# Optimization experiments

Measured on AMD Instinct MI355X. Metric: run time of the kernel, lower is better.

## Reference

```python
import jax, jax.numpy as jnp
import numpy as np

EPS = 0.1
SHAPE = (1, 1, 96, 96)  # [B, C, H, W]


def setup_inputs() -> dict:
    key = jax.random.key(0)
    x = jax.random.normal(key, SHAPE, dtype=jnp.float32)
    return {"x": x}


def reference(x):
    eps = EPS
    B, C, H, W = x.shape
    N = C * H * W  # max possible new error terms; buffer grows to 1 + N slots

    # clip the eps-ball into [0, 1]: bias shifts, error radius shrinks
    r_low = jax.nn.relu(eps - x) * 0.5
    r_high = jax.nn.relu(x - (1.0 - eps)) * 0.5
    bias = x + r_low - r_high                  # zonotope center, [B,C,H,W]
    err = eps - r_low - r_high                 # per-pixel error magnitude

    ef = err.reshape(N)
    cond = ef >= 0                             # which pixels get an error term
    # stream compaction: k-th true condition -> error-term slot 1+k (slot 0 = bias)
    slot = jnp.cumsum(cond.astype(jnp.int32))  # 1-based compacted index
    err_idx = jnp.where(cond, slot, N + 1)     # out-of-range -> dropped

    f, i, j = jnp.unravel_index(jnp.arange(N), (C, H, W))

    zono = jnp.zeros((B, 1 + N, C, H, W), dtype=x.dtype)
    zono = zono.at[0, 0].set(bias[0])
    zono = zono.at[0, err_idx, f, i, j].set(ef, mode='drop')
    return zono
```

## Files before the change

### kernel.cpp

```cpp
#include <hip/hip_runtime.h>

#define NPIX 9216
#define NROWS (NPIX + 1)
#define ROW4 (NPIX / 4)
#define EPSV 0.1f

typedef float f32x4 __attribute__((ext_vector_type(4)));

__global__ __launch_bounds__(1024) void finish_kernel(const float* __restrict__ x,
                                                      float* __restrict__ out) {
    __shared__ int wsum[16];
    const int tid  = threadIdx.x;
    const int lane = tid & 63;
    const int wid  = tid >> 6;
    const int base = tid * 9;

    float e_loc[9];
    int   c_loc[9];
    int   cnt = 0;
#pragma unroll
    for (int k = 0; k < 9; ++k) {
        const float xv     = x[base + k];
        const float r_low  = fmaxf(EPSV - xv, 0.0f) * 0.5f;
        const float r_high = fmaxf(xv - (1.0f - EPSV), 0.0f) * 0.5f;
        const float e      = EPSV - r_low - r_high;
        e_loc[k] = e;
        c_loc[k] = (e >= 0.0f) ? 1 : 0;
        cnt += c_loc[k];
    }

    int v = cnt;
#pragma unroll
    for (int off = 1; off < 64; off <<= 1) {
        const int t = __shfl_up(v, off, 64);
        if (lane >= off) v += t;
    }
    if (lane == 63) wsum[wid] = v;
    __syncthreads();

    int woff = 0;
#pragma unroll
    for (int w = 0; w < 16; ++w) woff += (w < wid) ? wsum[w] : 0;

    int slot = woff + v - cnt;
#pragma unroll
    for (int k = 0; k < 9; ++k) {
        if (c_loc[k]) {
            ++slot;
            out[(long long)slot * NPIX + (base + k)] = e_loc[k];
        }
    }

    const f32x4* x4 = reinterpret_cast<const f32x4*>(x);
    f32x4* o4 = reinterpret_cast<f32x4*>(out);
#pragma unroll
    for (int it = 0; it < 3; ++it) {
        const int c4 = tid + it * 1024;
        if (c4 < ROW4) {
            const f32x4 xv = x4[c4];
            f32x4 o;
#pragma unroll
            for (int d = 0; d < 4; ++d) {
                const float vv = xv[d];
                o[d] = vv + fmaxf(EPSV - vv, 0.0f) * 0.5f
                          - fmaxf(vv - (1.0f - EPSV), 0.0f) * 0.5f;
            }
            o4[c4] = o;
        }
    }
}

extern "C" void kernel_launch(void* const* d_in, const int* in_sizes, int n_in,
                              void* d_out, int out_size, void* d_ws, size_t ws_size,
                              hipStream_t stream) {
    const float* x = (const float*)d_in[0];
    float* out = (float*)d_out;

    hipMemsetAsync(d_out, 0, (size_t)out_size * sizeof(float), stream);
    finish_kernel<<<1, 1024, 0, stream>>>(x, out);
}
```

Measured before the change: 62.61 us.

## Replace memset plus scatter with a single dense write kernel over output rows

A single-block prep kernel now computes the compacted slot for each pixel and records a (pixel index, error value) pair per output row in workspace. A wide grid kernel then writes every output element exactly once: the bias row, or zeros with the one error value placed in each error row. This removes the separate full-buffer memset and the scattered stores that followed it. In exchange it adds a second launch and relies on a hand-written streaming store kernel matching the memset's bandwidth on a very large output.

Result: faster. 60.53 us (-3.3%).

```diff
diff --git a/kernel.cpp b/kernel.cpp
--- a/kernel.cpp
+++ b/kernel.cpp
@@ -3,17 +3,20 @@
 #define NPIX 9216
 #define NROWS (NPIX + 1)
 #define ROW4 (NPIX / 4)
+#define BLKS_PER_ROW 9
 #define EPSV 0.1f
 
 typedef float f32x4 __attribute__((ext_vector_type(4)));
 
-__global__ __launch_bounds__(1024) void finish_kernel(const float* __restrict__ x,
-                                                      float* __restrict__ out) {
+__global__ __launch_bounds__(1024) void prep_kernel(const float* __restrict__ x,
+                                                    int2* __restrict__ iv) {
     __shared__ int wsum[16];
     const int tid  = threadIdx.x;
     const int lane = tid & 63;
     const int wid  = tid >> 6;
     const int base = tid * 9;
+
+    for (int s = tid; s < NROWS; s += 1024) iv[s] = make_int2(-1, 0);
 
     float e_loc[9];
     int   c_loc[9];
@@ -47,27 +50,38 @@
     for (int k = 0; k < 9; ++k) {
         if (c_loc[k]) {
             ++slot;
-            out[(long long)slot * NPIX + (base + k)] = e_loc[k];
+            iv[slot] = make_int2(base + k, __float_as_int(e_loc[k]));
         }
     }
+}
 
-    const f32x4* x4 = reinterpret_cast<const f32x4*>(x);
-    f32x4* o4 = reinterpret_cast<f32x4*>(out);
+__global__ __launch_bounds__(256) void write_kernel(const float* __restrict__ x,
+                                                    const int2* __restrict__ iv,
+                                                    f32x4* __restrict__ out) {
+    const int bid  = blockIdx.x;
+    const int row  = bid / BLKS_PER_ROW;
+    const int sub  = bid - row * BLKS_PER_ROW;
+    const int col4 = sub * 256 + threadIdx.x;
+
+    f32x4 o;
+    if (row == 0) {
+        const f32x4 xv = reinterpret_cast<const f32x4*>(x)[col4];
 #pragma unroll
-    for (int it = 0; it < 3; ++it) {
-        const int c4 = tid + it * 1024;
-        if (c4 < ROW4) {
-            const f32x4 xv = x4[c4];
-            f32x4 o;
-#pragma unroll
-            for (int d = 0; d < 4; ++d) {
-                const float vv = xv[d];
-                o[d] = vv + fmaxf(EPSV - vv, 0.0f) * 0.5f
-                          - fmaxf(vv - (1.0f - EPSV), 0.0f) * 0.5f;
-            }
-            o4[c4] = o;
+        for (int d = 0; d < 4; ++d) {
+            const float v = xv[d];
+            o[d] = v + fmaxf(EPSV - v, 0.0f) * 0.5f
+                     - fmaxf(v - (1.0f - EPSV), 0.0f) * 0.5f;
         }
+    } else {
+        const int2 p = iv[row];
+        const float e = __int_as_float(p.y);
+        const int col = col4 * 4;
+        o.x = (p.x == col)     ? e : 0.0f;
+        o.y = (p.x == col + 1) ? e : 0.0f;
+        o.z = (p.x == col + 2) ? e : 0.0f;
+        o.w = (p.x == col + 3) ? e : 0.0f;
     }
+    out[(long long)row * ROW4 + col4] = o;
 }
 
 extern "C" void kernel_launch(void* const* d_in, const int* in_sizes, int n_in,
@@ -75,7 +89,8 @@
                               hipStream_t stream) {
     const float* x = (const float*)d_in[0];
     float* out = (float*)d_out;
+    int2* iv = (int2*)d_ws;
 
-    hipMemsetAsync(d_out, 0, (size_t)out_size * sizeof(float), stream);
-    finish_kernel<<<1, 1024, 0, stream>>>(x, out);
+    prep_kernel<<<1, 1024, 0, stream>>>(x, iv);
+    write_kernel<<<NROWS * BLKS_PER_ROW, 256, 0, stream>>>(x, iv, (f32x4*)out);
 }
```

## Replace memset plus scatter with compacted index list and single full-row write pass

Applied to the files above, without the earlier changes.

A single-block prep kernel now records, for each error-term slot, the pixel index and error value in a workspace array, and writes the bias row. A wide second kernel then writes every error row in full with vector stores, placing the value in its column and zeros elsewhere. This removes the separate memset pass and the strided scatter, so the large output is written only once. It adds a second kernel launch and a small workspace dependency.

Result: slower. 70.73 us (+13.0%).

```diff
diff --git a/kernel.cpp b/kernel.cpp
--- a/kernel.cpp
+++ b/kernel.cpp
@@ -5,15 +5,21 @@
 #define ROW4 (NPIX / 4)
 #define EPSV 0.1f
 
+#define SPT 3
+#define BLKS_PER_ROW 3
+
 typedef float f32x4 __attribute__((ext_vector_type(4)));
 
-__global__ __launch_bounds__(1024) void finish_kernel(const float* __restrict__ x,
-                                                      float* __restrict__ out) {
+__global__ __launch_bounds__(1024) void prep_kernel(const float* __restrict__ x,
+                                                    int2* __restrict__ iv,
+                                                    f32x4* __restrict__ out) {
     __shared__ int wsum[16];
     const int tid  = threadIdx.x;
     const int lane = tid & 63;
     const int wid  = tid >> 6;
     const int base = tid * 9;
+
+    for (int s = tid; s < NROWS; s += 1024) iv[s] = make_int2(-1, 0);
 
     float e_loc[9];
     int   c_loc[9];
@@ -47,12 +53,11 @@
     for (int k = 0; k < 9; ++k) {
         if (c_loc[k]) {
             ++slot;
-            out[(long long)slot * NPIX + (base + k)] = e_loc[k];
+            iv[slot] = make_int2(base + k, __float_as_int(e_loc[k]));
         }
     }
 
     const f32x4* x4 = reinterpret_cast<const f32x4*>(x);
-    f32x4* o4 = reinterpret_cast<f32x4*>(out);
 #pragma unroll
     for (int it = 0; it < 3; ++it) {
         const int c4 = tid + it * 1024;
@@ -65,8 +70,30 @@
                 o[d] = vv + fmaxf(EPSV - vv, 0.0f) * 0.5f
                           - fmaxf(vv - (1.0f - EPSV), 0.0f) * 0.5f;
             }
-            o4[c4] = o;
+            out[c4] = o;
         }
+    }
+}
+
+__global__ __launch_bounds__(256) void write_kernel(const int2* __restrict__ iv,
+                                                    f32x4* __restrict__ out) {
+    const int bid = blockIdx.x;
+    const int row = bid / BLKS_PER_ROW + 1;
+    const int sub = bid - (row - 1) * BLKS_PER_ROW;
+
+    const int2 p  = iv[row];
+    const float e = __int_as_float(p.y);
+
+    f32x4* orow = out + (long long)row * ROW4 + sub * (256 * SPT) + threadIdx.x;
+#pragma unroll
+    for (int it = 0; it < SPT; ++it) {
+        const int col = (sub * (256 * SPT) + it * 256 + threadIdx.x) * 4;
+        f32x4 o;
+        o.x = (p.x == col)     ? e : 0.0f;
+        o.y = (p.x == col + 1) ? e : 0.0f;
+        o.z = (p.x == col + 2) ? e : 0.0f;
+        o.w = (p.x == col + 3) ? e : 0.0f;
+        orow[it * 256] = o;
     }
 }
 
@@ -75,7 +102,8 @@
                               hipStream_t stream) {
     const float* x = (const float*)d_in[0];
     float* out = (float*)d_out;
+    int2* iv = (int2*)d_ws;
 
-    hipMemsetAsync(d_out, 0, (size_t)out_size * sizeof(float), stream);
-    finish_kernel<<<1, 1024, 0, stream>>>(x, out);
+    prep_kernel<<<1, 1024, 0, stream>>>(x, iv, (f32x4*)out);
+    write_kernel<<<NPIX * BLKS_PER_ROW, 256, 0, stream>>>(iv, (f32x4*)out);
 }
```
